# Optimization experiments

Hardware: AMD Instinct MI355X
Metric: run time of the kernel (lower is better)

Reference implementation:

```python
import jax, jax.numpy as jnp
import numpy as np

B = 64            # batch size (number of segments)
PTS = 4096        # points per segment
N = B * PTS       # total points
OBS = 128
ACT = 5
HID = 256
LAT = 64
CTX = 128
TEMP = 1.0
LOG2PIE = float(np.log(2.0 * np.pi * np.e))


def _p(key, shape, scale=0.02):
    return (scale * jax.random.normal(key, shape)).astype(jnp.float32)


def setup_inputs() -> dict:
    key = jax.random.key(0)
    ks = jax.random.split(key, 20)
    inp = {
        'obs': jax.random.normal(ks[0], (N, OBS), dtype=jnp.float32),
        'action': jax.random.normal(ks[1], (B, ACT), dtype=jnp.float32),
        'coh_scalar': jax.random.normal(ks[2], (B, 1), dtype=jnp.float32),
        'coh_spatial': jax.random.normal(ks[3], (N,), dtype=jnp.float32),
        'h_prev': jnp.zeros((B, HID), jnp.float32),
        'z_prev': jnp.zeros((B, LAT), jnp.float32),
        'batch': jnp.repeat(jnp.arange(B, dtype=jnp.int64), PTS),
    }
    xin = LAT + ACT + 1  # GRU input: [z_prev, action, coh_scalar]
    inp['W_ih'] = _p(ks[4], (3 * HID, xin)); inp['b_ih'] = jnp.zeros((3 * HID,), jnp.float32)
    inp['W_hh'] = _p(ks[5], (3 * HID, HID)); inp['b_hh'] = jnp.zeros((3 * HID,), jnp.float32)
    inp['W_prior'] = _p(ks[6], (2 * LAT, HID)); inp['b_prior'] = jnp.zeros((2 * LAT,), jnp.float32)
    inp['W_post'] = _p(ks[7], (2 * LAT, HID + OBS)); inp['b_post'] = jnp.zeros((2 * LAT,), jnp.float32)
    inp['W_ae1'] = _p(ks[8], (256, OBS)); inp['b_ae1'] = jnp.zeros((256,), jnp.float32)
    inp['W_ae2'] = _p(ks[9], (OBS, 256)); inp['b_ae2'] = jnp.zeros((OBS,), jnp.float32)
    inp['W_c1'] = _p(ks[10], (512, HID + LAT + OBS)); inp['b_c1'] = jnp.zeros((512,), jnp.float32)
    inp['W_c2'] = _p(ks[11], (CTX, 512)); inp['b_c2'] = jnp.zeros((CTX,), jnp.float32)
    return inp


def _forward(obs, action, coh_scalar, coh_spatial, h_prev, z_prev, batch,
             W_ih, b_ih, W_hh, b_hh, W_prior, b_prior, W_post, b_post,
             W_ae1, b_ae1, W_ae2, b_ae2, W_c1, b_c1, W_c2, b_c2):
    # --- segment mean of obs (the hot scatter-reduce) ---
    counts = jax.ops.segment_sum(jnp.ones((N,), obs.dtype), batch, num_segments=B)
    obs_sum = jax.ops.segment_sum(obs, batch, num_segments=B)            # (B, OBS)
    obs_agg = obs_sum / jnp.maximum(counts, 1.0)[:, None]

    # --- RSSM: GRU cell over [z_prev, action, coh_scalar] ---
    x = jnp.concatenate([z_prev, action, coh_scalar], axis=-1)           # (B, LAT+ACT+1)
    gi = x @ W_ih.T + b_ih
    gh = h_prev @ W_hh.T + b_hh
    gi_r, gi_z, gi_n = jnp.split(gi, 3, axis=-1)
    gh_r, gh_z, gh_n = jnp.split(gh, 3, axis=-1)
    r = jax.nn.sigmoid(gi_r + gh_r)
    u = jax.nn.sigmoid(gi_z + gh_z)
    n = jnp.tanh(gi_n + r * gh_n)
    h = (1.0 - u) * n + u * h_prev                                       # (B, HID)

    prior = h @ W_prior.T + b_prior
    mu_p, logvar_p = jnp.split(prior, 2, axis=-1)
    post = jnp.concatenate([h, obs_agg], axis=-1) @ W_post.T + b_post
    mu_q, logvar_q = jnp.split(post, 2, axis=-1)
    z = mu_q                                                             # deterministic baseline (B, LAT)

    # --- priority: entropy-based uncertainty, per-segment softmax ---
    uncertainty = 0.5 * jnp.sum(logvar_q + LOG2PIE, axis=-1)             # (B,)
    priority = coh_spatial * uncertainty[batch]                          # (N,)
    s = priority / TEMP
    m = jax.ops.segment_max(s, batch, num_segments=B)
    e = jnp.exp(s - m[batch])
    denom = jax.ops.segment_sum(e, batch, num_segments=B)
    priority_norm = e / jnp.maximum(denom, 1e-12)[batch]                 # (N,)

    # --- attended aggregation (second scatter-reduce) ---
    obs_attended = jax.ops.segment_sum(obs * priority_norm[:, None], batch, num_segments=B)  # (B, OBS)
    obs_enc = jax.nn.relu(obs_attended @ W_ae1.T + b_ae1) @ W_ae2.T + b_ae2                  # (B, OBS)

    ctx_in = jnp.concatenate([h, z, obs_enc], axis=-1)                   # (B, HID+LAT+OBS)
    context = jax.nn.relu(ctx_in @ W_c1.T + b_c1) @ W_c2.T + b_c2        # (B, CTX)
    return h, z, context, priority, priority_norm, uncertainty


def reference(obs, action, coh_scalar, coh_spatial, h_prev, z_prev, batch,
              W_ih, b_ih, W_hh, b_hh, W_prior, b_prior, W_post, b_post,
              W_ae1, b_ae1, W_ae2, b_ae2, W_c1, b_c1, W_c2, b_c2):
    return _forward(obs, action, coh_scalar, coh_spatial, h_prev, z_prev, batch,
                    W_ih, b_ih, W_hh, b_hh, W_prior, b_prior, W_post, b_post,
                    W_ae1, b_ae1, W_ae2, b_ae2, W_c1, b_c1, W_c2, b_c2)
```

## Files before the change

kernel.cpp:

```cpp
#include <hip/hip_runtime.h>
#include <math.h>

#define BB   64
#define PTS  4096
#define NTOT (BB * PTS)
#define OBS  128
#define ACT  5
#define HID  256
#define LAT  64
#define CTX  128
#define LOG2PIE 2.8378770664093453f

#define OFF_H   0
#define OFF_Z   (BB * HID)
#define OFF_CTX (OFF_Z + BB * LAT)
#define OFF_PRI (OFF_CTX + BB * CTX)
#define OFF_PN  (OFF_PRI + NTOT)
#define OFF_UNC (OFF_PN + NTOT)

#define CHUNKS 32
#define RPC    (PTS / CHUNKS)

__device__ __forceinline__ float wsum(float v) {
    #pragma unroll
    for (int off = 32; off > 0; off >>= 1) v += __shfl_xor(v, off, 64);
    return v;
}
__device__ __forceinline__ float wmax(float v) {
    #pragma unroll
    for (int off = 32; off > 0; off >>= 1) v = fmaxf(v, __shfl_xor(v, off, 64));
    return v;
}
__device__ __forceinline__ float sigmoidf_(float x) { return 1.f / (1.f + expf(-x)); }

__global__ __launch_bounds__(256) void phase1_kernel(
        const float* __restrict__ obs, float* __restrict__ part,
        const float* __restrict__ action, const float* __restrict__ coh_scalar,
        const float* __restrict__ h_prev, const float* __restrict__ z_prev,
        const float* __restrict__ W_ih, const float* __restrict__ b_ih,
        const float* __restrict__ W_hh, const float* __restrict__ b_hh,
        float* __restrict__ out) {
    __shared__ float4 lds[256];
    int t = threadIdx.x;
    if (blockIdx.x < BB * CHUNKS) {
        int blk = blockIdx.x;
        int b = blk >> 5, chunk = blk & 31;
        int c4 = t & 31, rg = t >> 5;
        const float4* obs4 = (const float4*)obs;
        size_t row0 = (size_t)b * PTS + (size_t)chunk * RPC;
        float4 acc = make_float4(0.f, 0.f, 0.f, 0.f);
        #pragma unroll
        for (int i = 0; i < RPC / 8; ++i) {
            float4 v = obs4[(row0 + rg + 8 * i) * (OBS / 4) + c4];
            acc.x += v.x; acc.y += v.y; acc.z += v.z; acc.w += v.w;
        }
        lds[t] = acc;
        __syncthreads();
        if (t < 32) {
            float4 s = lds[t];
            #pragma unroll
            for (int k = 1; k < 8; ++k) {
                float4 v = lds[t + 32 * k];
                s.x += v.x; s.y += v.y; s.z += v.z; s.w += v.w;
            }
            ((float4*)part)[(size_t)blk * 32 + t] = s;
        }
    } else {
        int wid = (blockIdx.x - BB * CHUNKS) * 4 + (t >> 6);
        int lane = t & 63;
        int b = wid >> 8, j = wid & 255;

        float x0 = z_prev[b * LAT + lane];
        float x1 = 0.f;
        if (lane < ACT) x1 = action[b * ACT + lane];
        else if (lane == ACT) x1 = coh_scalar[b];
        float hp0 = h_prev[b * HID + lane];
        float hp1 = h_prev[b * HID + lane + 64];
        float hp2 = h_prev[b * HID + lane + 128];
        float hp3 = h_prev[b * HID + lane + 192];

        const float* wir = W_ih + (size_t)j * 70;
        const float* wiz = W_ih + (size_t)(HID + j) * 70;
        const float* win = W_ih + (size_t)(2 * HID + j) * 70;
        const float* whr = W_hh + (size_t)j * HID;
        const float* whz = W_hh + (size_t)(HID + j) * HID;
        const float* whn = W_hh + (size_t)(2 * HID + j) * HID;

        float sr = wir[lane] * x0;
        float sz = wiz[lane] * x0;
        float sn = win[lane] * x0;
        if (lane < 6) {
            sr = fmaf(wir[lane + 64], x1, sr);
            sz = fmaf(wiz[lane + 64], x1, sz);
            sn = fmaf(win[lane + 64], x1, sn);
        }
        sr = fmaf(whr[lane], hp0, sr); sr = fmaf(whr[lane + 64], hp1, sr);
        sr = fmaf(whr[lane + 128], hp2, sr); sr = fmaf(whr[lane + 192], hp3, sr);
        sz = fmaf(whz[lane], hp0, sz); sz = fmaf(whz[lane + 64], hp1, sz);
        sz = fmaf(whz[lane + 128], hp2, sz); sz = fmaf(whz[lane + 192], hp3, sz);
        float sh = whn[lane] * hp0;
        sh = fmaf(whn[lane + 64], hp1, sh);
        sh = fmaf(whn[lane + 128], hp2, sh);
        sh = fmaf(whn[lane + 192], hp3, sh);

        sr = wsum(sr); sz = wsum(sz); sn = wsum(sn); sh = wsum(sh);
        if (lane == 0) {
            float r = sigmoidf_(sr + b_ih[j] + b_hh[j]);
            float u = sigmoidf_(sz + b_ih[HID + j] + b_hh[HID + j]);
            float n = tanhf(sn + b_ih[2 * HID + j] + r * (sh + b_hh[2 * HID + j]));
            float h = (1.f - u) * n + u * h_prev[b * HID + j];
            out[OFF_H + b * HID + j] = h;
        }
    }
}

__global__ __launch_bounds__(256) void post_kernel(
        const float* __restrict__ part,
        const float* __restrict__ W_post, const float* __restrict__ b_post,
        float* __restrict__ out, float* __restrict__ lv) {
    int blk = blockIdx.x;
    int b = blk >> 5, rg = blk & 31;
    int t = threadIdx.x, w = t >> 6, lane = t & 63;
    __shared__ float4 st[256];
    __shared__ float aggs[128];
    __shared__ float hs[256];

    const float4* ap4 = (const float4*)part;
    {
        int c4 = t & 31, cg = t >> 5;
        float4 a = ap4[((size_t)(b * CHUNKS + cg)) * 32 + c4];
        #pragma unroll
        for (int k = 1; k < 4; ++k) {
            float4 v = ap4[((size_t)(b * CHUNKS + cg + 8 * k)) * 32 + c4];
            a.x += v.x; a.y += v.y; a.z += v.z; a.w += v.w;
        }
        st[t] = a;
    }
    hs[t] = out[OFF_H + b * HID + t];
    __syncthreads();
    if (t < 32) {
        float4 s = st[t];
        #pragma unroll
        for (int k = 1; k < 8; ++k) {
            float4 v = st[t + 32 * k];
            s.x += v.x; s.y += v.y; s.z += v.z; s.w += v.w;
        }
        const float sc = 1.0f / PTS;
        aggs[4 * t + 0] = s.x * sc;
        aggs[4 * t + 1] = s.y * sc;
        aggs[4 * t + 2] = s.z * sc;
        aggs[4 * t + 3] = s.w * sc;
    }
    __syncthreads();

    int row = rg * 4 + w;
    const float* wr = W_post + (size_t)row * (HID + OBS);
    float s = wr[lane] * hs[lane];
    s = fmaf(wr[lane + 64],  hs[lane + 64],  s);
    s = fmaf(wr[lane + 128], hs[lane + 128], s);
    s = fmaf(wr[lane + 192], hs[lane + 192], s);
    s = fmaf(wr[lane + 256], aggs[lane],      s);
    s = fmaf(wr[lane + 320], aggs[lane + 64], s);
    s = wsum(s);
    if (lane == 0) {
        s += b_post[row];
        if (row < LAT) out[OFF_Z + b * LAT + row] = s;
        else           lv[b * LAT + (row - LAT)] = s;
    }
}

__global__ __launch_bounds__(1024) void softmax_kernel(
        const float* __restrict__ coh_spatial, const float* __restrict__ lv,
        float* __restrict__ out) {
    int b = blockIdx.x, t = threadIdx.x;
    int w = t >> 6, lane = t & 63;
    __shared__ float sv[PTS];
    __shared__ float red[16];
    __shared__ float uS;
    if (w == 0) {
        float v = lv[b * LAT + lane];
        v = wsum(v);
        if (lane == 0) {
            float u = 0.5f * v + 32.0f * LOG2PIE;
            uS = u;
            out[OFF_UNC + b] = u;
        }
    }
    __syncthreads();
    float u = uS;
    int base = b * PTS;
    float lmax = -INFINITY;
    #pragma unroll
    for (int i = t; i < PTS; i += 1024) {
        float s = coh_spatial[base + i] * u;
        sv[i] = s;
        out[OFF_PRI + base + i] = s;
        lmax = fmaxf(lmax, s);
    }
    lmax = wmax(lmax);
    if (lane == 0) red[w] = lmax;
    __syncthreads();
    float m = red[0];
    #pragma unroll
    for (int k = 1; k < 16; ++k) m = fmaxf(m, red[k]);
    __syncthreads();
    float lsum = 0.f;
    #pragma unroll
    for (int i = t; i < PTS; i += 1024) {
        float e = expf(sv[i] - m);
        sv[i] = e;
        lsum += e;
    }
    lsum = wsum(lsum);
    if (lane == 0) red[w] = lsum;
    __syncthreads();
    float d = 0.f;
    #pragma unroll
    for (int k = 0; k < 16; ++k) d += red[k];
    float inv = 1.f / fmaxf(d, 1e-12f);
    #pragma unroll
    for (int i = t; i < PTS; i += 1024) {
        out[OFF_PN + base + i] = sv[i] * inv;
    }
}

__global__ __launch_bounds__(256) void attn_part_kernel(
        const float* __restrict__ obs, const float* __restrict__ pn,
        float* __restrict__ att_part) {
    int blk = blockIdx.x;
    int b = blk >> 5, chunk = blk & 31;
    int t = threadIdx.x, c4 = t & 31, rg = t >> 5;
    const float4* obs4 = (const float4*)obs;
    size_t row0 = (size_t)b * PTS + (size_t)chunk * RPC;
    float4 acc = make_float4(0.f, 0.f, 0.f, 0.f);
    #pragma unroll
    for (int i = 0; i < RPC / 8; ++i) {
        size_t r = row0 + rg + 8 * i;
        float wgt = pn[r];
        float4 v = obs4[r * (OBS / 4) + c4];
        acc.x = fmaf(v.x, wgt, acc.x);
        acc.y = fmaf(v.y, wgt, acc.y);
        acc.z = fmaf(v.z, wgt, acc.z);
        acc.w = fmaf(v.w, wgt, acc.w);
    }
    __shared__ float4 lds[256];
    lds[t] = acc;
    __syncthreads();
    if (t < 32) {
        float4 s = lds[t];
        #pragma unroll
        for (int k = 1; k < 8; ++k) {
            float4 v = lds[t + 32 * k];
            s.x += v.x; s.y += v.y; s.z += v.z; s.w += v.w;
        }
        ((float4*)att_part)[(size_t)blk * 32 + t] = s;
    }
}

__global__ __launch_bounds__(1024) void head_kernel(
        const float* __restrict__ att_part,
        const float* __restrict__ W_ae1, const float* __restrict__ b_ae1,
        const float* __restrict__ W_ae2, const float* __restrict__ b_ae2,
        const float* __restrict__ W_c1,  const float* __restrict__ b_c1,
        const float* __restrict__ W_c2,  const float* __restrict__ b_c2,
        float* __restrict__ out) {
    int b = blockIdx.x, t = threadIdx.x;
    int w = t >> 6, lane = t & 63;
    __shared__ float4 red4[1024];
    __shared__ float att[128];
    __shared__ float h1[256];
    __shared__ float ctxin[448];
    __shared__ float c1v[512];

    {
        int c4 = t & 31, chunk = t >> 5;
        const float4* ap4 = (const float4*)att_part;
        red4[t] = ap4[((size_t)(b * CHUNKS + chunk)) * 32 + c4];
    }
    if (t < 256) ctxin[t] = out[OFF_H + b * HID + t];
    else if (t < 320) ctxin[t] = out[OFF_Z + b * LAT + (t - 256)];
    __syncthreads();
    #pragma unroll
    for (int s = 16; s > 0; s >>= 1) {
        if ((t >> 5) < s) {
            float4 v = red4[t + 32 * s];
            red4[t].x += v.x; red4[t].y += v.y; red4[t].z += v.z; red4[t].w += v.w;
        }
        __syncthreads();
    }
    if (t < 32) {
        float4 v = red4[t];
        att[4 * t] = v.x; att[4 * t + 1] = v.y; att[4 * t + 2] = v.z; att[4 * t + 3] = v.w;
    }
    __syncthreads();

    {
        float x0 = att[lane], x1 = att[lane + 64];
        #pragma unroll
        for (int g = 0; g < 4; ++g) {
            int r0 = w * 16 + g * 4;
            const float* w0 = W_ae1 + (size_t)(r0 + 0) * OBS;
            const float* w1 = W_ae1 + (size_t)(r0 + 1) * OBS;
            const float* w2 = W_ae1 + (size_t)(r0 + 2) * OBS;
            const float* w3 = W_ae1 + (size_t)(r0 + 3) * OBS;
            float a0 = fmaf(w0[lane + 64], x1, w0[lane] * x0);
            float a1 = fmaf(w1[lane + 64], x1, w1[lane] * x0);
            float a2 = fmaf(w2[lane + 64], x1, w2[lane] * x0);
            float a3 = fmaf(w3[lane + 64], x1, w3[lane] * x0);
            a0 = wsum(a0); a1 = wsum(a1); a2 = wsum(a2); a3 = wsum(a3);
            if (lane == 0) {
                h1[r0]     = fmaxf(a0 + b_ae1[r0],     0.f);
                h1[r0 + 1] = fmaxf(a1 + b_ae1[r0 + 1], 0.f);
                h1[r0 + 2] = fmaxf(a2 + b_ae1[r0 + 2], 0.f);
                h1[r0 + 3] = fmaxf(a3 + b_ae1[r0 + 3], 0.f);
            }
        }
    }
    __syncthreads();

    {
        float x0 = h1[lane], x1 = h1[lane + 64], x2 = h1[lane + 128], x3 = h1[lane + 192];
        #pragma unroll
        for (int g = 0; g < 2; ++g) {
            int r0 = w * 8 + g * 4;
            const float* w0 = W_ae2 + (size_t)(r0 + 0) * 256;
            const float* w1 = W_ae2 + (size_t)(r0 + 1) * 256;
            const float* w2 = W_ae2 + (size_t)(r0 + 2) * 256;
            const float* w3 = W_ae2 + (size_t)(r0 + 3) * 256;
            float a0 = w0[lane] * x0, a1 = w1[lane] * x0, a2 = w2[lane] * x0, a3 = w3[lane] * x0;
            a0 = fmaf(w0[lane + 64], x1, a0);  a1 = fmaf(w1[lane + 64], x1, a1);
            a2 = fmaf(w2[lane + 64], x1, a2);  a3 = fmaf(w3[lane + 64], x1, a3);
            a0 = fmaf(w0[lane + 128], x2, a0); a1 = fmaf(w1[lane + 128], x2, a1);
            a2 = fmaf(w2[lane + 128], x2, a2); a3 = fmaf(w3[lane + 128], x2, a3);
            a0 = fmaf(w0[lane + 192], x3, a0); a1 = fmaf(w1[lane + 192], x3, a1);
            a2 = fmaf(w2[lane + 192], x3, a2); a3 = fmaf(w3[lane + 192], x3, a3);
            a0 = wsum(a0); a1 = wsum(a1); a2 = wsum(a2); a3 = wsum(a3);
            if (lane == 0) {
                ctxin[320 + r0]     = a0 + b_ae2[r0];
                ctxin[320 + r0 + 1] = a1 + b_ae2[r0 + 1];
                ctxin[320 + r0 + 2] = a2 + b_ae2[r0 + 2];
                ctxin[320 + r0 + 3] = a3 + b_ae2[r0 + 3];
            }
        }
    }
    __syncthreads();

    {
        float x0 = ctxin[lane],        x1 = ctxin[lane + 64],  x2 = ctxin[lane + 128];
        float x3 = ctxin[lane + 192],  x4 = ctxin[lane + 256], x5 = ctxin[lane + 320];
        float x6 = ctxin[lane + 384];
        #pragma unroll
        for (int g = 0; g < 8; ++g) {
            int r0 = w * 32 + g * 4;
            const float* w0 = W_c1 + (size_t)(r0 + 0) * 448;
            const float* w1 = W_c1 + (size_t)(r0 + 1) * 448;
            const float* w2 = W_c1 + (size_t)(r0 + 2) * 448;
            const float* w3 = W_c1 + (size_t)(r0 + 3) * 448;
            float a0 = w0[lane] * x0, a1 = w1[lane] * x0, a2 = w2[lane] * x0, a3 = w3[lane] * x0;
            a0 = fmaf(w0[lane + 64], x1, a0);  a1 = fmaf(w1[lane + 64], x1, a1);
            a2 = fmaf(w2[lane + 64], x1, a2);  a3 = fmaf(w3[lane + 64], x1, a3);
            a0 = fmaf(w0[lane + 128], x2, a0); a1 = fmaf(w1[lane + 128], x2, a1);
            a2 = fmaf(w2[lane + 128], x2, a2); a3 = fmaf(w3[lane + 128], x2, a3);
            a0 = fmaf(w0[lane + 192], x3, a0); a1 = fmaf(w1[lane + 192], x3, a1);
            a2 = fmaf(w2[lane + 192], x3, a2); a3 = fmaf(w3[lane + 192], x3, a3);
            a0 = fmaf(w0[lane + 256], x4, a0); a1 = fmaf(w1[lane + 256], x4, a1);
            a2 = fmaf(w2[lane + 256], x4, a2); a3 = fmaf(w3[lane + 256], x4, a3);
            a0 = fmaf(w0[lane + 320], x5, a0); a1 = fmaf(w1[lane + 320], x5, a1);
            a2 = fmaf(w2[lane + 320], x5, a2); a3 = fmaf(w3[lane + 320], x5, a3);
            a0 = fmaf(w0[lane + 384], x6, a0); a1 = fmaf(w1[lane + 384], x6, a1);
            a2 = fmaf(w2[lane + 384], x6, a2); a3 = fmaf(w3[lane + 384], x6, a3);
            a0 = wsum(a0); a1 = wsum(a1); a2 = wsum(a2); a3 = wsum(a3);
            if (lane == 0) {
                c1v[r0]     = fmaxf(a0 + b_c1[r0],     0.f);
                c1v[r0 + 1] = fmaxf(a1 + b_c1[r0 + 1], 0.f);
                c1v[r0 + 2] = fmaxf(a2 + b_c1[r0 + 2], 0.f);
                c1v[r0 + 3] = fmaxf(a3 + b_c1[r0 + 3], 0.f);
            }
        }
    }
    __syncthreads();

    {
        float x0 = c1v[lane],       x1 = c1v[lane + 64],  x2 = c1v[lane + 128], x3 = c1v[lane + 192];
        float x4 = c1v[lane + 256], x5 = c1v[lane + 320], x6 = c1v[lane + 384], x7 = c1v[lane + 448];
        #pragma unroll
        for (int g = 0; g < 2; ++g) {
            int r0 = w * 8 + g * 4;
            const float* w0 = W_c2 + (size_t)(r0 + 0) * 512;
            const float* w1 = W_c2 + (size_t)(r0 + 1) * 512;
            const float* w2 = W_c2 + (size_t)(r0 + 2) * 512;
            const float* w3 = W_c2 + (size_t)(r0 + 3) * 512;
            float a0 = w0[lane] * x0, a1 = w1[lane] * x0, a2 = w2[lane] * x0, a3 = w3[lane] * x0;
            a0 = fmaf(w0[lane + 64], x1, a0);  a1 = fmaf(w1[lane + 64], x1, a1);
            a2 = fmaf(w2[lane + 64], x1, a2);  a3 = fmaf(w3[lane + 64], x1, a3);
            a0 = fmaf(w0[lane + 128], x2, a0); a1 = fmaf(w1[lane + 128], x2, a1);
            a2 = fmaf(w2[lane + 128], x2, a2); a3 = fmaf(w3[lane + 128], x2, a3);
            a0 = fmaf(w0[lane + 192], x3, a0); a1 = fmaf(w1[lane + 192], x3, a1);
            a2 = fmaf(w2[lane + 192], x3, a2); a3 = fmaf(w3[lane + 192], x3, a3);
            a0 = fmaf(w0[lane + 256], x4, a0); a1 = fmaf(w1[lane + 256], x4, a1);
            a2 = fmaf(w2[lane + 256], x4, a2); a3 = fmaf(w3[lane + 256], x4, a3);
            a0 = fmaf(w0[lane + 320], x5, a0); a1 = fmaf(w1[lane + 320], x5, a1);
            a2 = fmaf(w2[lane + 320], x5, a2); a3 = fmaf(w3[lane + 320], x5, a3);
            a0 = fmaf(w0[lane + 384], x6, a0); a1 = fmaf(w1[lane + 384], x6, a1);
            a2 = fmaf(w2[lane + 384], x6, a2); a3 = fmaf(w3[lane + 384], x6, a3);
            a0 = fmaf(w0[lane + 448], x7, a0); a1 = fmaf(w1[lane + 448], x7, a1);
            a2 = fmaf(w2[lane + 448], x7, a2); a3 = fmaf(w3[lane + 448], x7, a3);
            a0 = wsum(a0); a1 = wsum(a1); a2 = wsum(a2); a3 = wsum(a3);
            if (lane == 0) {
                float* dst = out + OFF_CTX + b * CTX;
                dst[r0]     = a0 + b_c2[r0];
                dst[r0 + 1] = a1 + b_c2[r0 + 1];
                dst[r0 + 2] = a2 + b_c2[r0 + 2];
                dst[r0 + 3] = a3 + b_c2[r0 + 3];
            }
        }
    }
}

extern "C" void kernel_launch(void* const* d_in, const int* in_sizes, int n_in,
                              void* d_out, int out_size, void* d_ws, size_t ws_size,
                              hipStream_t stream) {
    const float* obs         = (const float*)d_in[0];
    const float* action      = (const float*)d_in[1];
    const float* coh_scalar  = (const float*)d_in[2];
    const float* coh_spatial = (const float*)d_in[3];
    const float* h_prev      = (const float*)d_in[4];
    const float* z_prev      = (const float*)d_in[5];
    const float* W_ih   = (const float*)d_in[7];
    const float* b_ih   = (const float*)d_in[8];
    const float* W_hh   = (const float*)d_in[9];
    const float* b_hh   = (const float*)d_in[10];
    const float* W_post = (const float*)d_in[13];
    const float* b_post = (const float*)d_in[14];
    const float* W_ae1  = (const float*)d_in[15];
    const float* b_ae1  = (const float*)d_in[16];
    const float* W_ae2  = (const float*)d_in[17];
    const float* b_ae2  = (const float*)d_in[18];
    const float* W_c1   = (const float*)d_in[19];
    const float* b_c1   = (const float*)d_in[20];
    const float* W_c2   = (const float*)d_in[21];
    const float* b_c2   = (const float*)d_in[22];

    float* out = (float*)d_out;
    float* part     = (float*)d_ws;
    float* att_part = part + BB * CHUNKS * OBS;
    float* lv       = att_part + BB * CHUNKS * OBS;

    phase1_kernel<<<BB * CHUNKS + BB * HID / 4, 256, 0, stream>>>(
        obs, part, action, coh_scalar, h_prev, z_prev, W_ih, b_ih, W_hh, b_hh, out);
    post_kernel<<<BB * 32, 256, 0, stream>>>(part, W_post, b_post, out, lv);
    softmax_kernel<<<BB, 1024, 0, stream>>>(coh_spatial, lv, out);
    attn_part_kernel<<<BB * CHUNKS, 256, 0, stream>>>(obs, out + OFF_PN, att_part);
    head_kernel<<<BB, 1024, 0, stream>>>(att_part, W_ae1, b_ae1, W_ae2, b_ae2,
                                         W_c1, b_c1, W_c2, b_c2, out);
}
```

Before: 295.3 us.

## Fuse four phase kernels into one cooperative persistent kernel with grid syncs

Merges the obs segment-sum plus GRU, the posterior projection, the softmax and the attended partial-sum kernels into one cooperative kernel of 512 blocks that separates phases with grid.sync. Each block now handles four obs chunks and four GRU rows per wave. The aim is to cut kernel launch gaps and per-kernel tail effects. In exchange the softmax phase runs on only 64 blocks of 256 threads, leaving most of the grid idle at that stage, and each grid barrier adds its own cost.

```diff
diff --git a/kernel.cpp b/kernel.cpp
--- a/kernel.cpp
+++ b/kernel.cpp
@@ -1,5 +1,8 @@
 #include <hip/hip_runtime.h>
+#include <hip/hip_cooperative_groups.h>
 #include <math.h>
+
+namespace cg = cooperative_groups;
 
 #define BB   64
 #define PTS  4096
@@ -20,6 +23,7 @@
 
 #define CHUNKS 32
 #define RPC    (PTS / CHUNKS)
+#define GRID_C 512
 
 __device__ __forceinline__ float wsum(float v) {
     #pragma unroll
@@ -33,43 +37,52 @@
 }
 __device__ __forceinline__ float sigmoidf_(float x) { return 1.f / (1.f + expf(-x)); }
 
-__global__ __launch_bounds__(256) void phase1_kernel(
+__global__ __launch_bounds__(256, 4) void coop_kernel(
         const float* __restrict__ obs, float* __restrict__ part,
         const float* __restrict__ action, const float* __restrict__ coh_scalar,
         const float* __restrict__ h_prev, const float* __restrict__ z_prev,
         const float* __restrict__ W_ih, const float* __restrict__ b_ih,
         const float* __restrict__ W_hh, const float* __restrict__ b_hh,
-        float* __restrict__ out) {
-    __shared__ float4 lds[256];
-    int t = threadIdx.x;
-    if (blockIdx.x < BB * CHUNKS) {
-        int blk = blockIdx.x;
-        int b = blk >> 5, chunk = blk & 31;
+        const float* __restrict__ W_post, const float* __restrict__ b_post,
+        const float* __restrict__ coh_spatial, float* __restrict__ lv,
+        float* __restrict__ att_part, float* __restrict__ out) {
+    cg::grid_group grid = cg::this_grid();
+    __shared__ __align__(16) float smem[4160];
+    int t = threadIdx.x, w = t >> 6, lane = t & 63;
+    int blk = blockIdx.x;
+
+    {
+        float4* l4 = (float4*)smem;
+        const float4* obs4 = (const float4*)obs;
         int c4 = t & 31, rg = t >> 5;
-        const float4* obs4 = (const float4*)obs;
-        size_t row0 = (size_t)b * PTS + (size_t)chunk * RPC;
-        float4 acc = make_float4(0.f, 0.f, 0.f, 0.f);
-        #pragma unroll
-        for (int i = 0; i < RPC / 8; ++i) {
-            float4 v = obs4[(row0 + rg + 8 * i) * (OBS / 4) + c4];
-            acc.x += v.x; acc.y += v.y; acc.z += v.z; acc.w += v.w;
-        }
-        lds[t] = acc;
-        __syncthreads();
-        if (t < 32) {
-            float4 s = lds[t];
+        for (int cc = 0; cc < 4; ++cc) {
+            int cid = blk * 4 + cc;
+            int b = cid >> 5, chunk = cid & 31;
+            size_t row0 = (size_t)b * PTS + (size_t)chunk * RPC;
+            float4 acc = make_float4(0.f, 0.f, 0.f, 0.f);
             #pragma unroll
-            for (int k = 1; k < 8; ++k) {
-                float4 v = lds[t + 32 * k];
-                s.x += v.x; s.y += v.y; s.z += v.z; s.w += v.w;
-            }
-            ((float4*)part)[(size_t)blk * 32 + t] = s;
-        }
-    } else {
-        int wid = (blockIdx.x - BB * CHUNKS) * 4 + (t >> 6);
-        int lane = t & 63;
-        int b = wid >> 8, j = wid & 255;
-
+            for (int i = 0; i < RPC / 8; ++i) {
+                float4 v = obs4[(row0 + rg + 8 * i) * (OBS / 4) + c4];
+                acc.x += v.x; acc.y += v.y; acc.z += v.z; acc.w += v.w;
+            }
+            l4[t] = acc;
+            __syncthreads();
+            if (t < 32) {
+                float4 s = l4[t];
+                #pragma unroll
+                for (int k = 1; k < 8; ++k) {
+                    float4 v = l4[t + 32 * k];
+                    s.x += v.x; s.y += v.y; s.z += v.z; s.w += v.w;
+                }
+                ((float4*)part)[(size_t)cid * 32 + t] = s;
+            }
+            __syncthreads();
+        }
+    }
+    for (int it = 0; it < 2; ++it) {
+        int wid = (blk * 4 + w) + 2048 * it;
+        int b = wid >> 6;
+        int j0 = (wid & 63) * 4;
         float x0 = z_prev[b * LAT + lane];
         float x1 = 0.f;
         if (lane < ACT) x1 = action[b * ACT + lane];
@@ -78,182 +91,184 @@
         float hp1 = h_prev[b * HID + lane + 64];
         float hp2 = h_prev[b * HID + lane + 128];
         float hp3 = h_prev[b * HID + lane + 192];
-
-        const float* wir = W_ih + (size_t)j * 70;
-        const float* wiz = W_ih + (size_t)(HID + j) * 70;
-        const float* win = W_ih + (size_t)(2 * HID + j) * 70;
-        const float* whr = W_hh + (size_t)j * HID;
-        const float* whz = W_hh + (size_t)(HID + j) * HID;
-        const float* whn = W_hh + (size_t)(2 * HID + j) * HID;
-
-        float sr = wir[lane] * x0;
-        float sz = wiz[lane] * x0;
-        float sn = win[lane] * x0;
-        if (lane < 6) {
-            sr = fmaf(wir[lane + 64], x1, sr);
-            sz = fmaf(wiz[lane + 64], x1, sz);
-            sn = fmaf(win[lane + 64], x1, sn);
-        }
-        sr = fmaf(whr[lane], hp0, sr); sr = fmaf(whr[lane + 64], hp1, sr);
-        sr = fmaf(whr[lane + 128], hp2, sr); sr = fmaf(whr[lane + 192], hp3, sr);
-        sz = fmaf(whz[lane], hp0, sz); sz = fmaf(whz[lane + 64], hp1, sz);
-        sz = fmaf(whz[lane + 128], hp2, sz); sz = fmaf(whz[lane + 192], hp3, sz);
-        float sh = whn[lane] * hp0;
-        sh = fmaf(whn[lane + 64], hp1, sh);
-        sh = fmaf(whn[lane + 128], hp2, sh);
-        sh = fmaf(whn[lane + 192], hp3, sh);
-
-        sr = wsum(sr); sz = wsum(sz); sn = wsum(sn); sh = wsum(sh);
+        #pragma unroll
+        for (int jj = 0; jj < 4; ++jj) {
+            int j = j0 + jj;
+            const float* wir = W_ih + (size_t)j * 70;
+            const float* wiz = W_ih + (size_t)(HID + j) * 70;
+            const float* win = W_ih + (size_t)(2 * HID + j) * 70;
+            const float* whr = W_hh + (size_t)j * HID;
+            const float* whz = W_hh + (size_t)(HID + j) * HID;
+            const float* whn = W_hh + (size_t)(2 * HID + j) * HID;
+            float sr = wir[lane] * x0, sz = wiz[lane] * x0, sn = win[lane] * x0;
+            if (lane < 6) {
+                sr = fmaf(wir[lane + 64], x1, sr);
+                sz = fmaf(wiz[lane + 64], x1, sz);
+                sn = fmaf(win[lane + 64], x1, sn);
+            }
+            sr = fmaf(whr[lane], hp0, sr); sr = fmaf(whr[lane + 64], hp1, sr);
+            sr = fmaf(whr[lane + 128], hp2, sr); sr = fmaf(whr[lane + 192], hp3, sr);
+            sz = fmaf(whz[lane], hp0, sz); sz = fmaf(whz[lane + 64], hp1, sz);
+            sz = fmaf(whz[lane + 128], hp2, sz); sz = fmaf(whz[lane + 192], hp3, sz);
+            float sh = whn[lane] * hp0;
+            sh = fmaf(whn[lane + 64], hp1, sh);
+            sh = fmaf(whn[lane + 128], hp2, sh);
+            sh = fmaf(whn[lane + 192], hp3, sh);
+            sr = wsum(sr); sz = wsum(sz); sn = wsum(sn); sh = wsum(sh);
+            if (lane == 0) {
+                float r = sigmoidf_(sr + b_ih[j] + b_hh[j]);
+                float u = sigmoidf_(sz + b_ih[HID + j] + b_hh[HID + j]);
+                float n = tanhf(sn + b_ih[2 * HID + j] + r * (sh + b_hh[2 * HID + j]));
+                out[OFF_H + b * HID + j] = (1.f - u) * n + u * h_prev[b * HID + j];
+            }
+        }
+    }
+    __threadfence();
+    grid.sync();
+
+    {
+        float4* st  = (float4*)smem;
+        float* hs   = smem + 1024;
+        float* aggs = smem + 1280;
+        int b = blk >> 3, sub = blk & 7;
+        {
+            int c4 = t & 31, cgp = t >> 5;
+            const float4* ap4 = (const float4*)part;
+            float4 a = ap4[((size_t)(b * CHUNKS + cgp)) * 32 + c4];
+            #pragma unroll
+            for (int k = 1; k < 4; ++k) {
+                float4 v = ap4[((size_t)(b * CHUNKS + cgp + 8 * k)) * 32 + c4];
+                a.x += v.x; a.y += v.y; a.z += v.z; a.w += v.w;
+            }
+            st[t] = a;
+        }
+        hs[t] = out[OFF_H + b * HID + t];
+        __syncthreads();
+        if (t < 32) {
+            float4 s = st[t];
+            #pragma unroll
+            for (int k = 1; k < 8; ++k) {
+                float4 v = st[t + 32 * k];
+                s.x += v.x; s.y += v.y; s.z += v.z; s.w += v.w;
+            }
+            const float sc = 1.0f / PTS;
+            aggs[4 * t + 0] = s.x * sc; aggs[4 * t + 1] = s.y * sc;
+            aggs[4 * t + 2] = s.z * sc; aggs[4 * t + 3] = s.w * sc;
+        }
+        __syncthreads();
+        int r0 = sub * 16 + w * 4;
+        const float* w0 = W_post + (size_t)r0 * 384;
+        const float* w1 = w0 + 384;
+        const float* w2 = w0 + 768;
+        const float* w3 = w0 + 1152;
+        float a0 = w0[lane] * hs[lane], a1 = w1[lane] * hs[lane];
+        float a2 = w2[lane] * hs[lane], a3 = w3[lane] * hs[lane];
+        a0 = fmaf(w0[lane + 64],  hs[lane + 64],  a0); a1 = fmaf(w1[lane + 64],  hs[lane + 64],  a1);
+        a2 = fmaf(w2[lane + 64],  hs[lane + 64],  a2); a3 = fmaf(w3[lane + 64],  hs[lane + 64],  a3);
+        a0 = fmaf(w0[lane + 128], hs[lane + 128], a0); a1 = fmaf(w1[lane + 128], hs[lane + 128], a1);
+        a2 = fmaf(w2[lane + 128], hs[lane + 128], a2); a3 = fmaf(w3[lane + 128], hs[lane + 128], a3);
+        a0 = fmaf(w0[lane + 192], hs[lane + 192], a0); a1 = fmaf(w1[lane + 192], hs[lane + 192], a1);
+        a2 = fmaf(w2[lane + 192], hs[lane + 192], a2); a3 = fmaf(w3[lane + 192], hs[lane + 192], a3);
+        a0 = fmaf(w0[lane + 256], aggs[lane],      a0); a1 = fmaf(w1[lane + 256], aggs[lane],      a1);
+        a2 = fmaf(w2[lane + 256], aggs[lane],      a2); a3 = fmaf(w3[lane + 256], aggs[lane],      a3);
+        a0 = fmaf(w0[lane + 320], aggs[lane + 64], a0); a1 = fmaf(w1[lane + 320], aggs[lane + 64], a1);
+        a2 = fmaf(w2[lane + 320], aggs[lane + 64], a2); a3 = fmaf(w3[lane + 320], aggs[lane + 64], a3);
+        a0 = wsum(a0); a1 = wsum(a1); a2 = wsum(a2); a3 = wsum(a3);
         if (lane == 0) {
-            float r = sigmoidf_(sr + b_ih[j] + b_hh[j]);
-            float u = sigmoidf_(sz + b_ih[HID + j] + b_hh[HID + j]);
-            float n = tanhf(sn + b_ih[2 * HID + j] + r * (sh + b_hh[2 * HID + j]));
-            float h = (1.f - u) * n + u * h_prev[b * HID + j];
-            out[OFF_H + b * HID + j] = h;
-        }
-    }
-}
-
-__global__ __launch_bounds__(256) void post_kernel(
-        const float* __restrict__ part,
-        const float* __restrict__ W_post, const float* __restrict__ b_post,
-        float* __restrict__ out, float* __restrict__ lv) {
-    int blk = blockIdx.x;
-    int b = blk >> 5, rg = blk & 31;
-    int t = threadIdx.x, w = t >> 6, lane = t & 63;
-    __shared__ float4 st[256];
-    __shared__ float aggs[128];
-    __shared__ float hs[256];
-
-    const float4* ap4 = (const float4*)part;
-    {
-        int c4 = t & 31, cg = t >> 5;
-        float4 a = ap4[((size_t)(b * CHUNKS + cg)) * 32 + c4];
-        #pragma unroll
-        for (int k = 1; k < 4; ++k) {
-            float4 v = ap4[((size_t)(b * CHUNKS + cg + 8 * k)) * 32 + c4];
-            a.x += v.x; a.y += v.y; a.z += v.z; a.w += v.w;
-        }
-        st[t] = a;
-    }
-    hs[t] = out[OFF_H + b * HID + t];
-    __syncthreads();
-    if (t < 32) {
-        float4 s = st[t];
-        #pragma unroll
-        for (int k = 1; k < 8; ++k) {
-            float4 v = st[t + 32 * k];
-            s.x += v.x; s.y += v.y; s.z += v.z; s.w += v.w;
-        }
-        const float sc = 1.0f / PTS;
-        aggs[4 * t + 0] = s.x * sc;
-        aggs[4 * t + 1] = s.y * sc;
-        aggs[4 * t + 2] = s.z * sc;
-        aggs[4 * t + 3] = s.w * sc;
-    }
-    __syncthreads();
-
-    int row = rg * 4 + w;
-    const float* wr = W_post + (size_t)row * (HID + OBS);
-    float s = wr[lane] * hs[lane];
-    s = fmaf(wr[lane + 64],  hs[lane + 64],  s);
-    s = fmaf(wr[lane + 128], hs[lane + 128], s);
-    s = fmaf(wr[lane + 192], hs[lane + 192], s);
-    s = fmaf(wr[lane + 256], aggs[lane],      s);
-    s = fmaf(wr[lane + 320], aggs[lane + 64], s);
-    s = wsum(s);
-    if (lane == 0) {
-        s += b_post[row];
-        if (row < LAT) out[OFF_Z + b * LAT + row] = s;
-        else           lv[b * LAT + (row - LAT)] = s;
-    }
-}
-
-__global__ __launch_bounds__(1024) void softmax_kernel(
-        const float* __restrict__ coh_spatial, const float* __restrict__ lv,
-        float* __restrict__ out) {
-    int b = blockIdx.x, t = threadIdx.x;
-    int w = t >> 6, lane = t & 63;
-    __shared__ float sv[PTS];
-    __shared__ float red[16];
-    __shared__ float uS;
-    if (w == 0) {
-        float v = lv[b * LAT + lane];
-        v = wsum(v);
-        if (lane == 0) {
-            float u = 0.5f * v + 32.0f * LOG2PIE;
-            uS = u;
-            out[OFF_UNC + b] = u;
-        }
-    }
-    __syncthreads();
-    float u = uS;
-    int base = b * PTS;
-    float lmax = -INFINITY;
-    #pragma unroll
-    for (int i = t; i < PTS; i += 1024) {
-        float s = coh_spatial[base + i] * u;
-        sv[i] = s;
-        out[OFF_PRI + base + i] = s;
-        lmax = fmaxf(lmax, s);
-    }
-    lmax = wmax(lmax);
-    if (lane == 0) red[w] = lmax;
-    __syncthreads();
-    float m = red[0];
-    #pragma unroll
-    for (int k = 1; k < 16; ++k) m = fmaxf(m, red[k]);
-    __syncthreads();
-    float lsum = 0.f;
-    #pragma unroll
-    for (int i = t; i < PTS; i += 1024) {
-        float e = expf(sv[i] - m);
-        sv[i] = e;
-        lsum += e;
-    }
-    lsum = wsum(lsum);
-    if (lane == 0) red[w] = lsum;
-    __syncthreads();
-    float d = 0.f;
-    #pragma unroll
-    for (int k = 0; k < 16; ++k) d += red[k];
-    float inv = 1.f / fmaxf(d, 1e-12f);
-    #pragma unroll
-    for (int i = t; i < PTS; i += 1024) {
-        out[OFF_PN + base + i] = sv[i] * inv;
-    }
-}
-
-__global__ __launch_bounds__(256) void attn_part_kernel(
-        const float* __restrict__ obs, const float* __restrict__ pn,
-        float* __restrict__ att_part) {
-    int blk = blockIdx.x;
-    int b = blk >> 5, chunk = blk & 31;
-    int t = threadIdx.x, c4 = t & 31, rg = t >> 5;
-    const float4* obs4 = (const float4*)obs;
-    size_t row0 = (size_t)b * PTS + (size_t)chunk * RPC;
-    float4 acc = make_float4(0.f, 0.f, 0.f, 0.f);
-    #pragma unroll
-    for (int i = 0; i < RPC / 8; ++i) {
-        size_t r = row0 + rg + 8 * i;
-        float wgt = pn[r];
-        float4 v = obs4[r * (OBS / 4) + c4];
-        acc.x = fmaf(v.x, wgt, acc.x);
-        acc.y = fmaf(v.y, wgt, acc.y);
-        acc.z = fmaf(v.z, wgt, acc.z);
-        acc.w = fmaf(v.w, wgt, acc.w);
-    }
-    __shared__ float4 lds[256];
-    lds[t] = acc;
-    __syncthreads();
-    if (t < 32) {
-        float4 s = lds[t];
-        #pragma unroll
-        for (int k = 1; k < 8; ++k) {
-            float4 v = lds[t + 32 * k];
-            s.x += v.x; s.y += v.y; s.z += v.z; s.w += v.w;
-        }
-        ((float4*)att_part)[(size_t)blk * 32 + t] = s;
+            a0 += b_post[r0]; a1 += b_post[r0 + 1]; a2 += b_post[r0 + 2]; a3 += b_post[r0 + 3];
+            if (r0 < LAT) {
+                float* dst = out + OFF_Z + b * LAT + r0;
+                dst[0] = a0; dst[1] = a1; dst[2] = a2; dst[3] = a3;
+            } else {
+                float* dst = lv + b * LAT + (r0 - LAT);
+                dst[0] = a0; dst[1] = a1; dst[2] = a2; dst[3] = a3;
+            }
+        }
+    }
+    __threadfence();
+    grid.sync();
+
+    if (blk < BB) {
+        int b = blk;
+        float* sv  = smem;
+        float* red = smem + 4096;
+        float* uS  = smem + 4100;
+        if (w == 0) {
+            float v = lv[b * LAT + lane];
+            v = wsum(v);
+            if (lane == 0) {
+                float u = 0.5f * v + 32.0f * LOG2PIE;
+                *uS = u;
+                out[OFF_UNC + b] = u;
+            }
+        }
+        __syncthreads();
+        float u = *uS;
+        int base = b * PTS;
+        float lmax = -INFINITY;
+        #pragma unroll
+        for (int i = t; i < PTS; i += 256) {
+            float s = coh_spatial[base + i] * u;
+            sv[i] = s;
+            out[OFF_PRI + base + i] = s;
+            lmax = fmaxf(lmax, s);
+        }
+        lmax = wmax(lmax);
+        if (lane == 0) red[w] = lmax;
+        __syncthreads();
+        float m = fmaxf(fmaxf(red[0], red[1]), fmaxf(red[2], red[3]));
+        __syncthreads();
+        float lsum = 0.f;
+        #pragma unroll
+        for (int i = t; i < PTS; i += 256) {
+            float e = expf(sv[i] - m);
+            sv[i] = e;
+            lsum += e;
+        }
+        lsum = wsum(lsum);
+        if (lane == 0) red[w] = lsum;
+        __syncthreads();
+        float inv = 1.f / fmaxf(red[0] + red[1] + red[2] + red[3], 1e-12f);
+        #pragma unroll
+        for (int i = t; i < PTS; i += 256) {
+            out[OFF_PN + base + i] = sv[i] * inv;
+        }
+    }
+    __threadfence();
+    grid.sync();
+
+    {
+        float4* l4 = (float4*)smem;
+        const float4* obs4 = (const float4*)obs;
+        int c4 = t & 31, rg = t >> 5;
+        for (int cc = 0; cc < 4; ++cc) {
+            int cid = blk * 4 + cc;
+            int b = cid >> 5, chunk = cid & 31;
+            size_t row0 = (size_t)b * PTS + (size_t)chunk * RPC;
+            float4 acc = make_float4(0.f, 0.f, 0.f, 0.f);
+            #pragma unroll
+            for (int i = 0; i < RPC / 8; ++i) {
+                size_t r = row0 + rg + 8 * i;
+                float wg = out[OFF_PN + r];
+                float4 v = obs4[r * (OBS / 4) + c4];
+                acc.x = fmaf(v.x, wg, acc.x);
+                acc.y = fmaf(v.y, wg, acc.y);
+                acc.z = fmaf(v.z, wg, acc.z);
+                acc.w = fmaf(v.w, wg, acc.w);
+            }
+            __syncthreads();
+            l4[t] = acc;
+            __syncthreads();
+            if (t < 32) {
+                float4 s = l4[t];
+                #pragma unroll
+                for (int k = 1; k < 8; ++k) {
+                    float4 v = l4[t + 32 * k];
+                    s.x += v.x; s.y += v.y; s.z += v.z; s.w += v.w;
+                }
+                ((float4*)att_part)[(size_t)cid * 32 + t] = s;
+            }
+        }
     }
 }
 
@@ -346,8 +361,8 @@
     __syncthreads();
 
     {
-        float x0 = ctxin[lane],        x1 = ctxin[lane + 64],  x2 = ctxin[lane + 128];
-        float x3 = ctxin[lane + 192],  x4 = ctxin[lane + 256], x5 = ctxin[lane + 320];
+        float x0 = ctxin[lane],       x1 = ctxin[lane + 64],  x2 = ctxin[lane + 128];
+        float x3 = ctxin[lane + 192], x4 = ctxin[lane + 256], x5 = ctxin[lane + 320];
         float x6 = ctxin[lane + 384];
         #pragma unroll
         for (int g = 0; g < 8; ++g) {
@@ -441,16 +456,19 @@
     const float* W_c2   = (const float*)d_in[21];
     const float* b_c2   = (const float*)d_in[22];
 
-    float* out = (float*)d_out;
+    float* outp     = (float*)d_out;
     float* part     = (float*)d_ws;
     float* att_part = part + BB * CHUNKS * OBS;
     float* lv       = att_part + BB * CHUNKS * OBS;
 
-    phase1_kernel<<<BB * CHUNKS + BB * HID / 4, 256, 0, stream>>>(
-        obs, part, action, coh_scalar, h_prev, z_prev, W_ih, b_ih, W_hh, b_hh, out);
-    post_kernel<<<BB * 32, 256, 0, stream>>>(part, W_post, b_post, out, lv);
-    softmax_kernel<<<BB, 1024, 0, stream>>>(coh_spatial, lv, out);
-    attn_part_kernel<<<BB * CHUNKS, 256, 0, stream>>>(obs, out + OFF_PN, att_part);
+    void* kargs[] = {
+        (void*)&obs, (void*)&part, (void*)&action, (void*)&coh_scalar,
+        (void*)&h_prev, (void*)&z_prev, (void*)&W_ih, (void*)&b_ih,
+        (void*)&W_hh, (void*)&b_hh, (void*)&W_post, (void*)&b_post,
+        (void*)&coh_spatial, (void*)&lv, (void*)&att_part, (void*)&outp
+    };
+    hipLaunchCooperativeKernel(reinterpret_cast<void*>(coop_kernel),
+                               dim3(GRID_C), dim3(256), kargs, 0, stream);
     head_kernel<<<BB, 1024, 0, stream>>>(att_part, W_ae1, b_ae1, W_ae2, b_ae2,
-                                         W_c1, b_c1, W_c2, b_c2, out);
+                                         W_c1, b_c1, W_c2, b_c2, outp);
 }
```

Result: slower. 606.8 us (+105.5%).
